# Optimization experiments

Measured on AMD Instinct MI355X. Metric: run time of the kernel, lower is better.

The kernel has to match this reference:

```python
import jax, jax.numpy as jnp
import numpy as np

N, C_IN, F = 64, 1024, 20          # batch, backbone channels, grid size (640/32)
N_CLASSES = 80
A = 3                               # anchors in this layer (mask [6,7,8])
STRIDE = 32
C = N_CLASSES + 5                   # 85
C_OUT = A * C                       # 255
ANCHORS = np.array([[116.0, 90.0], [156.0, 198.0], [373.0, 326.0]], np.float32) / STRIDE


def setup_inputs() -> dict:
    key = jax.random.key(0)
    k1, k2 = jax.random.split(key)
    xin = jax.random.normal(k1, (N, C_IN, F, F), jnp.float32)
    conv_w = jax.random.normal(k2, (C_OUT, C_IN, 1, 1), jnp.float32) * 0.02
    conv_b = jnp.zeros((C_OUT,), jnp.float32)
    return {"xin": xin, "conv_w": conv_w, "conv_b": conv_b}


def reference(xin, conv_w, conv_b):
    anchors = jnp.asarray(ANCHORS, dtype=xin.dtype)  # [A, 2], grid units
    # 1x1 conv head: [N, C_OUT, F, F]
    out = jax.lax.conv_general_dilated(xin, conv_w, window_strides=(1, 1),
                                       padding="VALID")
    out = out + conv_b[None, :, None, None]
    # [N, A, C, F, F] -> [N, A, F(y), F(x), C]
    out = out.reshape(N, A, C, F, F).transpose(0, 1, 3, 4, 2)

    xy = jax.nn.sigmoid(out[..., :2])       # sigmoid on tx, ty
    wh = out[..., 2:4]                      # raw tw, th
    objcls = jax.nn.sigmoid(out[..., 4:])   # sigmoid on obj + classes

    grid = jnp.arange(F, dtype=xin.dtype)
    px = xy[..., 0] + grid[None, None, None, :]   # + x_shift (varies along last spatial dim)
    py = xy[..., 1] + grid[None, None, :, None]   # + y_shift
    pw = jnp.exp(wh[..., 0]) * anchors[:, 0].reshape(1, A, 1, 1)
    ph = jnp.exp(wh[..., 1]) * anchors[:, 1].reshape(1, A, 1, 1)

    boxes = jnp.stack([px, py, pw, ph], axis=-1) * STRIDE  # back to pixel coords
    pred = jnp.concatenate([boxes, objcls], axis=-1)       # [N, A, F, F, C]
    return pred.reshape(N, -1, C)                           # [N, A*F*F, C]
```

## Files before the change

kernel.cpp:

```cpp
#include <hip/hip_runtime.h>
#include <hip/hip_bf16.h>
#include <math.h>

#define CIN    1024
#define S_TOT  400
#define COUT   255
#define NCH    85
#define NIMG   64
#define SB     16
#define NTHR   256

#define LDS_BYTES 16384

typedef __attribute__((ext_vector_type(8))) short bf16x8;
typedef __attribute__((ext_vector_type(4))) float f32x4;

struct __attribute__((aligned(4))) f4u { float x, y, z, w; };

__device__ __forceinline__ int xOff(int s, int gl) {
    return (s << 10) + ((gl << 4) ^ (((s >> 1) & 7) << 4));
}

__device__ __forceinline__ unsigned pk2(float a, float b) {
    __hip_bfloat162 h;
    h.x = __float2bfloat16(a);
    h.y = __float2bfloat16(b);
    return *reinterpret_cast<unsigned*>(&h);
}

__device__ __forceinline__ float sigmoidf_(float v) {
    return 1.0f / (1.0f + expf(-v));
}

__global__ __launch_bounds__(256) void w_pre2(const float* __restrict__ w,
                                              unsigned short* __restrict__ wbf) {
    int gidx = blockIdx.x * 256 + threadIdx.x;
    int co = gidx & 255;
    int g  = gidx >> 8;
    union { unsigned short u[8]; bf16x8 v; } pk;
    if (co < COUT) {
        const float* src = w + (size_t)co * CIN + g * 8;
        #pragma unroll
        for (int j = 0; j < 8; ++j) {
            __hip_bfloat16 h = __float2bfloat16(src[j]);
            pk.u[j] = *reinterpret_cast<unsigned short*>(&h);
        }
    } else {
        #pragma unroll
        for (int j = 0; j < 8; ++j) pk.u[j] = 0;
    }
    *reinterpret_cast<bf16x8*>((char*)wbf + ((size_t)(g << 8) + co) * 16) = pk.v;
}

__global__ __launch_bounds__(NTHR, 4) void yolo_mfma3(
    const float* __restrict__ xin,
    const unsigned short* __restrict__ wbf,
    const float* __restrict__ bias,
    float* __restrict__ out)
{
    __shared__ __align__(16) char smem[LDS_BYTES];

    const int sb  = blockIdx.x * SB;
    const int n   = blockIdx.y;
    const int tid = threadIdx.x;
    const int lane = tid & 63;
    const int wid  = tid >> 6;
    const int llo  = lane & 15;
    const int lhi  = lane >> 4;

    const int gl_u = tid >> 2;
    const int sq_u = tid & 3;

    f32x4 acc[4] = {};

    for (int h = 0; h < 2; ++h) {
        if (h) __syncthreads();

        {
            const float* src = xin
                + ((size_t)n * CIN + h * 512 + gl_u * 8) * S_TOT
                + sb + 4 * sq_u;
            float4 cu[8];
            #pragma unroll
            for (int j = 0; j < 8; ++j) cu[j] = *(const float4*)(src + j * S_TOT);
            union { unsigned u[4]; bf16x8 v; } rr;
            #pragma unroll
            for (int r = 0; r < 4; ++r) {
                const float* cf = (const float*)cu;
                #pragma unroll
                for (int j = 0; j < 4; ++j)
                    rr.u[j] = pk2(cf[8 * j + r], cf[8 * j + 4 + r]);
                *(bf16x8*)(smem + xOff(4 * sq_u + r, gl_u)) = rr.v;
            }
        }
        __syncthreads();

        #pragma unroll 4
        for (int kk = 0; kk < 16; ++kk) {
            const int gA = (h * 16 + kk) * 4 + lhi;
            const int gl = kk * 4 + lhi;
            bf16x8 b = *(bf16x8*)(smem + xOff(llo, gl));
            #pragma unroll
            for (int mi = 0; mi < 4; ++mi) {
                const int co = wid * 64 + mi * 16 + llo;
                bf16x8 a = *(const bf16x8*)((const char*)wbf
                                            + ((size_t)(gA << 8) + co) * 16);
                acc[mi] = __builtin_amdgcn_mfma_f32_16x16x32_bf16(a, b, acc[mi], 0, 0, 0);
            }
        }
    }

    const float anchW[3] = {116.0f, 156.0f, 373.0f};
    const float anchH[3] = {90.0f, 198.0f, 326.0f};

    const int s = sb + llo;
    const float sx = (float)(s % 20);
    const float sy = (float)(s / 20);

    #pragma unroll
    for (int mi = 0; mi < 4; ++mi) {
        const int co0 = wid * 64 + mi * 16 + lhi * 4;
        const int aW  = co0 / NCH;
        const int c0  = co0 - aW * NCH;
        const bool whole = (c0 <= NCH - 4) && (co0 + 3 < COUT);
        float bv[4];
        #pragma unroll
        for (int r = 0; r < 4; ++r)
            bv[r] = (co0 + r < COUT) ? bias[co0 + r] : 0.0f;

        if (whole) {
            float r4[4];
            #pragma unroll
            for (int r = 0; r < 4; ++r) {
                const int c = c0 + r;
                const float v = acc[mi][r] + bv[r];
                float res;
                if (c == 0)      res = (sigmoidf_(v) + sx) * 32.0f;
                else if (c == 1) res = (sigmoidf_(v) + sy) * 32.0f;
                else if (c == 2) res = expf(v) * anchW[aW];
                else if (c == 3) res = expf(v) * anchH[aW];
                else             res = sigmoidf_(v);
                r4[r] = res;
            }
            f4u* p = (f4u*)(out + (size_t)n * 102000 + aW * 34000 + s * 85 + c0);
            f4u val = {r4[0], r4[1], r4[2], r4[3]};
            *p = val;
        } else {
            #pragma unroll
            for (int r = 0; r < 4; ++r) {
                const int co = co0 + r;
                if (co < COUT) {
                    const int a2 = co / NCH;
                    const int c  = co - a2 * NCH;
                    const float v = acc[mi][r] + bv[r];
                    float res;
                    if (c == 0)      res = (sigmoidf_(v) + sx) * 32.0f;
                    else if (c == 1) res = (sigmoidf_(v) + sy) * 32.0f;
                    else if (c == 2) res = expf(v) * anchW[a2];
                    else if (c == 3) res = expf(v) * anchH[a2];
                    else             res = sigmoidf_(v);
                    out[(size_t)n * 102000 + a2 * 34000 + s * 85 + c] = res;
                }
            }
        }
    }
}

extern "C" void kernel_launch(void* const* d_in, const int* in_sizes, int n_in,
                              void* d_out, int out_size, void* d_ws, size_t ws_size,
                              hipStream_t stream) {
    const float* xin  = (const float*)d_in[0];
    const float* w    = (const float*)d_in[1];
    const float* bias = (const float*)d_in[2];
    float* out = (float*)d_out;
    unsigned short* wbf = (unsigned short*)d_ws;

    w_pre2<<<128, 256, 0, stream>>>(w, wbf);
    yolo_mfma3<<<dim3(S_TOT / SB, NIMG), NTHR, 0, stream>>>(xin, wbf, bias, out);
}
```

Before: 77.23 us.

## Stage full K tile in LDS once and software-pipeline MFMA operand loads

The kernel now loads the whole 1024-channel input slice for the block into a 32 KB LDS buffer in one pass, where before it used two 512-channel halves separated by a barrier. The MFMA loop is restructured to prefetch the next iteration's LDS B operand and global weight A operands while the current MFMAs issue. This removes one barrier and is meant to hide weight-load latency behind compute. In exchange it doubles LDS per block, which may reduce occupancy, and it raises register pressure from the double-buffered operands.

Result: faster. 72.50 us (-6.1%).

```diff
diff --git a/kernel.cpp b/kernel.cpp
--- a/kernel.cpp
+++ b/kernel.cpp
@@ -10,15 +10,15 @@
 #define SB     16
 #define NTHR   256
 
-#define LDS_BYTES 16384
+#define LDS_BYTES 32768
 
 typedef __attribute__((ext_vector_type(8))) short bf16x8;
 typedef __attribute__((ext_vector_type(4))) float f32x4;
 
 struct __attribute__((aligned(4))) f4u { float x, y, z, w; };
 
-__device__ __forceinline__ int xOff(int s, int gl) {
-    return (s << 10) + ((gl << 4) ^ (((s >> 1) & 7) << 4));
+__device__ __forceinline__ int xOff(int s, int g) {
+    return (s << 11) + ((g << 4) ^ (((s >> 1) & 7) << 4));
 }
 
 __device__ __forceinline__ unsigned pk2(float a, float b) {
@@ -52,7 +52,7 @@
     *reinterpret_cast<bf16x8*>((char*)wbf + ((size_t)(g << 8) + co) * 16) = pk.v;
 }
 
-__global__ __launch_bounds__(NTHR, 4) void yolo_mfma3(
+__global__ __launch_bounds__(NTHR, 4) void yolo_mfma4(
     const float* __restrict__ xin,
     const unsigned short* __restrict__ wbf,
     const float* __restrict__ bias,
@@ -68,47 +68,55 @@
     const int llo  = lane & 15;
     const int lhi  = lane >> 4;
 
-    const int gl_u = tid >> 2;
-    const int sq_u = tid & 3;
+    #pragma unroll
+    for (int p = 0; p < 2; ++p) {
+        const int u   = p * 256 + tid;
+        const int g_u = u >> 2;
+        const int sq  = u & 3;
+        const float* src = xin + ((size_t)n * CIN + g_u * 8) * S_TOT + sb + 4 * sq;
+        float4 cu[8];
+        #pragma unroll
+        for (int j = 0; j < 8; ++j) cu[j] = *(const float4*)(src + j * S_TOT);
+        const float* cf = (const float*)cu;
+        #pragma unroll
+        for (int r = 0; r < 4; ++r) {
+            union { unsigned u4[4]; bf16x8 v; } rr;
+            #pragma unroll
+            for (int j = 0; j < 4; ++j)
+                rr.u4[j] = pk2(cf[8 * j + r], cf[8 * j + 4 + r]);
+            *(bf16x8*)(smem + xOff(4 * sq + r, g_u)) = rr.v;
+        }
+    }
+    __syncthreads();
 
     f32x4 acc[4] = {};
+    const char* wb = (const char*)wbf;
+    const int coB = wid * 64 + llo;
 
-    for (int h = 0; h < 2; ++h) {
-        if (h) __syncthreads();
+    bf16x8 b_c = *(bf16x8*)(smem + xOff(llo, lhi));
+    bf16x8 a_c[4];
+    #pragma unroll
+    for (int mi = 0; mi < 4; ++mi)
+        a_c[mi] = *(const bf16x8*)(wb + ((size_t)((lhi << 8) + coB + mi * 16)) * 16);
 
-        {
-            const float* src = xin
-                + ((size_t)n * CIN + h * 512 + gl_u * 8) * S_TOT
-                + sb + 4 * sq_u;
-            float4 cu[8];
-            #pragma unroll
-            for (int j = 0; j < 8; ++j) cu[j] = *(const float4*)(src + j * S_TOT);
-            union { unsigned u[4]; bf16x8 v; } rr;
-            #pragma unroll
-            for (int r = 0; r < 4; ++r) {
-                const float* cf = (const float*)cu;
-                #pragma unroll
-                for (int j = 0; j < 4; ++j)
-                    rr.u[j] = pk2(cf[8 * j + r], cf[8 * j + 4 + r]);
-                *(bf16x8*)(smem + xOff(4 * sq_u + r, gl_u)) = rr.v;
-            }
-        }
-        __syncthreads();
-
-        #pragma unroll 4
-        for (int kk = 0; kk < 16; ++kk) {
-            const int gA = (h * 16 + kk) * 4 + lhi;
-            const int gl = kk * 4 + lhi;
-            bf16x8 b = *(bf16x8*)(smem + xOff(llo, gl));
-            #pragma unroll
-            for (int mi = 0; mi < 4; ++mi) {
-                const int co = wid * 64 + mi * 16 + llo;
-                bf16x8 a = *(const bf16x8*)((const char*)wbf
-                                            + ((size_t)(gA << 8) + co) * 16);
-                acc[mi] = __builtin_amdgcn_mfma_f32_16x16x32_bf16(a, b, acc[mi], 0, 0, 0);
-            }
-        }
+    #pragma unroll 4
+    for (int kk = 0; kk < 31; ++kk) {
+        const int gn = (kk + 1) * 4 + lhi;
+        bf16x8 b_n = *(bf16x8*)(smem + xOff(llo, gn));
+        bf16x8 a_n[4];
+        #pragma unroll
+        for (int mi = 0; mi < 4; ++mi)
+            a_n[mi] = *(const bf16x8*)(wb + ((size_t)((gn << 8) + coB + mi * 16)) * 16);
+        #pragma unroll
+        for (int mi = 0; mi < 4; ++mi)
+            acc[mi] = __builtin_amdgcn_mfma_f32_16x16x32_bf16(a_c[mi], b_c, acc[mi], 0, 0, 0);
+        b_c = b_n;
+        #pragma unroll
+        for (int mi = 0; mi < 4; ++mi) a_c[mi] = a_n[mi];
     }
+    #pragma unroll
+    for (int mi = 0; mi < 4; ++mi)
+        acc[mi] = __builtin_amdgcn_mfma_f32_16x16x32_bf16(a_c[mi], b_c, acc[mi], 0, 0, 0);
 
     const float anchW[3] = {116.0f, 156.0f, 373.0f};
     const float anchH[3] = {90.0f, 198.0f, 326.0f};
@@ -176,5 +184,5 @@
     unsigned short* wbf = (unsigned short*)d_ws;
 
     w_pre2<<<128, 256, 0, stream>>>(w, wbf);
-    yolo_mfma3<<<dim3(S_TOT / SB, NIMG), NTHR, 0, stream>>>(xin, wbf, bias, out);
+    yolo_mfma4<<<dim3(S_TOT / SB, NIMG), NTHR, 0, stream>>>(xin, wbf, bias, out);
 }
```

## Flatten batch-spatial tiling to 64 positions per block with double-buffered LDS pipeline

Applied to the files above, without the earlier changes.

Flattens the batch and spatial dims into one index and gives each 512-thread block 64 positions across all output channels, so every weight fragment load feeds four MFMAs instead of one. The K dimension is split into four phases with double-buffered LDS: the next phase's global loads are issued before the current MFMAs and written to the other buffer afterwards, with one barrier per phase. This cuts weight traffic per block and overlaps input loads with compute. The cost is more registers (8 accumulators plus staging), 64KB of LDS and fewer, larger blocks. Tiles of 64 positions can span an image boundary, so the epilogue works out n and s for each position.

Result: faster. 69.22 us (-10.4%).

```diff
diff --git a/kernel.cpp b/kernel.cpp
--- a/kernel.cpp
+++ b/kernel.cpp
@@ -7,18 +7,23 @@
 #define COUT   255
 #define NCH    85
 #define NIMG   64
-#define SB     16
-#define NTHR   256
-
-#define LDS_BYTES 16384
+#define NFLAT  (NIMG * S_TOT)
+#define TS     64
+#define NTHR   512
+#define NPH    4
+#define KPH    256
+#define GPH    32
+
+#define XBUF_B    32768
+#define LDS_BYTES (2 * XBUF_B)
 
 typedef __attribute__((ext_vector_type(8))) short bf16x8;
 typedef __attribute__((ext_vector_type(4))) float f32x4;
 
 struct __attribute__((aligned(4))) f4u { float x, y, z, w; };
 
-__device__ __forceinline__ int xOff(int s, int gl) {
-    return (s << 10) + ((gl << 4) ^ (((s >> 1) & 7) << 4));
+__device__ __forceinline__ int xoff0(int s, int g) {
+    return (s << 9) + ((g << 4) ^ (((s ^ (s >> 3)) & 7) << 4));
 }
 
 __device__ __forceinline__ unsigned pk2(float a, float b) {
@@ -36,10 +41,10 @@
                                               unsigned short* __restrict__ wbf) {
     int gidx = blockIdx.x * 256 + threadIdx.x;
     int co = gidx & 255;
-    int g  = gidx >> 8;
+    int gg = gidx >> 8;
     union { unsigned short u[8]; bf16x8 v; } pk;
     if (co < COUT) {
-        const float* src = w + (size_t)co * CIN + g * 8;
+        const float* src = w + (size_t)co * CIN + gg * 8;
         #pragma unroll
         for (int j = 0; j < 8; ++j) {
             __hip_bfloat16 h = __float2bfloat16(src[j]);
@@ -49,10 +54,10 @@
         #pragma unroll
         for (int j = 0; j < 8; ++j) pk.u[j] = 0;
     }
-    *reinterpret_cast<bf16x8*>((char*)wbf + ((size_t)(g << 8) + co) * 16) = pk.v;
-}
-
-__global__ __launch_bounds__(NTHR, 4) void yolo_mfma3(
+    *reinterpret_cast<bf16x8*>((char*)wbf + ((size_t)(gg << 8) + co) * 16) = pk.v;
+}
+
+__global__ __launch_bounds__(NTHR, 4) void yolo_ws(
     const float* __restrict__ xin,
     const unsigned short* __restrict__ wbf,
     const float* __restrict__ bias,
@@ -60,52 +65,78 @@
 {
     __shared__ __align__(16) char smem[LDS_BYTES];
 
-    const int sb  = blockIdx.x * SB;
-    const int n   = blockIdx.y;
-    const int tid = threadIdx.x;
+    const int tile = blockIdx.x * TS;
+    const int tid  = threadIdx.x;
     const int lane = tid & 63;
-    const int wid  = tid >> 6;
+    const int w    = tid >> 6;
     const int llo  = lane & 15;
     const int lhi  = lane >> 4;
 
-    const int gl_u = tid >> 2;
-    const int sq_u = tid & 3;
-
-    f32x4 acc[4] = {};
-
-    for (int h = 0; h < 2; ++h) {
-        if (h) __syncthreads();
-
-        {
-            const float* src = xin
-                + ((size_t)n * CIN + h * 512 + gl_u * 8) * S_TOT
-                + sb + 4 * sq_u;
-            float4 cu[8];
-            #pragma unroll
-            for (int j = 0; j < 8; ++j) cu[j] = *(const float4*)(src + j * S_TOT);
-            union { unsigned u[4]; bf16x8 v; } rr;
+    const int flat_l = tile + 4 * llo;
+    const int n_l = flat_l / S_TOT;
+    const int s_l = flat_l - n_l * S_TOT;
+    const float* xbase = xin + (size_t)n_l * (CIN * S_TOT) + s_l;
+    const int ci_row = w * 32 + lhi * 8;
+    const int g_loc  = w * 4 + lhi;
+
+    f32x4 acc[2][4] = {};
+    union F4 { float4 v; float f[4]; };
+    F4 st[8];
+
+    {
+        const float* src = xbase + (size_t)ci_row * S_TOT;
+        #pragma unroll
+        for (int j = 0; j < 8; ++j) st[j].v = *(const float4*)(src + j * S_TOT);
+        #pragma unroll
+        for (int r = 0; r < 4; ++r) {
+            union { unsigned u4[4]; bf16x8 b; } rr;
+            #pragma unroll
+            for (int jj = 0; jj < 4; ++jj)
+                rr.u4[jj] = pk2(st[2 * jj].f[r], st[2 * jj + 1].f[r]);
+            *(bf16x8*)(smem + xoff0(4 * llo + r, g_loc)) = rr.b;
+        }
+    }
+
+    for (int p = 0; p < NPH; ++p) {
+        if (p + 1 < NPH) {
+            const float* src = xbase + (size_t)((p + 1) * KPH + ci_row) * S_TOT;
+            #pragma unroll
+            for (int j = 0; j < 8; ++j) st[j].v = *(const float4*)(src + j * S_TOT);
+        }
+        __builtin_amdgcn_sched_barrier(0);
+        asm volatile("s_waitcnt lgkmcnt(0)" ::: "memory");
+        __builtin_amdgcn_s_barrier();
+        __builtin_amdgcn_sched_barrier(0);
+
+        const char* xb = smem + (p & 1) * XBUF_B;
+        #pragma unroll
+        for (int step = 0; step < 8; ++step) {
+            const int gl = step * 4 + lhi;
+            bf16x8 bfr[4];
+            #pragma unroll
+            for (int ns = 0; ns < 4; ++ns)
+                bfr[ns] = *(const bf16x8*)(xb + xoff0(ns * 16 + llo, gl));
+            #pragma unroll
+            for (int mi = 0; mi < 2; ++mi) {
+                const int co = w * 32 + mi * 16 + llo;
+                bf16x8 a = *(const bf16x8*)((const char*)wbf
+                            + ((size_t)(((p * GPH + gl) << 8) + co)) * 16);
+                #pragma unroll
+                for (int ns = 0; ns < 4; ++ns)
+                    acc[mi][ns] = __builtin_amdgcn_mfma_f32_16x16x32_bf16(
+                        a, bfr[ns], acc[mi][ns], 0, 0, 0);
+            }
+        }
+
+        if (p + 1 < NPH) {
+            char* xb2 = smem + ((p + 1) & 1) * XBUF_B;
             #pragma unroll
             for (int r = 0; r < 4; ++r) {
-                const float* cf = (const float*)cu;
-                #pragma unroll
-                for (int j = 0; j < 4; ++j)
-                    rr.u[j] = pk2(cf[8 * j + r], cf[8 * j + 4 + r]);
-                *(bf16x8*)(smem + xOff(4 * sq_u + r, gl_u)) = rr.v;
-            }
-        }
-        __syncthreads();
-
-        #pragma unroll 4
-        for (int kk = 0; kk < 16; ++kk) {
-            const int gA = (h * 16 + kk) * 4 + lhi;
-            const int gl = kk * 4 + lhi;
-            bf16x8 b = *(bf16x8*)(smem + xOff(llo, gl));
-            #pragma unroll
-            for (int mi = 0; mi < 4; ++mi) {
-                const int co = wid * 64 + mi * 16 + llo;
-                bf16x8 a = *(const bf16x8*)((const char*)wbf
-                                            + ((size_t)(gA << 8) + co) * 16);
-                acc[mi] = __builtin_amdgcn_mfma_f32_16x16x32_bf16(a, b, acc[mi], 0, 0, 0);
+                union { unsigned u4[4]; bf16x8 b; } rr;
+                #pragma unroll
+                for (int jj = 0; jj < 4; ++jj)
+                    rr.u4[jj] = pk2(st[2 * jj].f[r], st[2 * jj + 1].f[r]);
+                *(bf16x8*)(xb2 + xoff0(4 * llo + r, g_loc)) = rr.b;
             }
         }
     }
@@ -113,13 +144,9 @@
     const float anchW[3] = {116.0f, 156.0f, 373.0f};
     const float anchH[3] = {90.0f, 198.0f, 326.0f};
 
-    const int s = sb + llo;
-    const float sx = (float)(s % 20);
-    const float sy = (float)(s / 20);
-
     #pragma unroll
-    for (int mi = 0; mi < 4; ++mi) {
-        const int co0 = wid * 64 + mi * 16 + lhi * 4;
+    for (int mi = 0; mi < 2; ++mi) {
+        const int co0 = w * 32 + mi * 16 + lhi * 4;
         const int aW  = co0 / NCH;
         const int c0  = co0 - aW * NCH;
         const bool whole = (c0 <= NCH - 4) && (co0 + 3 < COUT);
@@ -128,38 +155,46 @@
         for (int r = 0; r < 4; ++r)
             bv[r] = (co0 + r < COUT) ? bias[co0 + r] : 0.0f;
 
-        if (whole) {
-            float r4[4];
-            #pragma unroll
-            for (int r = 0; r < 4; ++r) {
-                const int c = c0 + r;
-                const float v = acc[mi][r] + bv[r];
-                float res;
-                if (c == 0)      res = (sigmoidf_(v) + sx) * 32.0f;
-                else if (c == 1) res = (sigmoidf_(v) + sy) * 32.0f;
-                else if (c == 2) res = expf(v) * anchW[aW];
-                else if (c == 3) res = expf(v) * anchH[aW];
-                else             res = sigmoidf_(v);
-                r4[r] = res;
-            }
-            f4u* p = (f4u*)(out + (size_t)n * 102000 + aW * 34000 + s * 85 + c0);
-            f4u val = {r4[0], r4[1], r4[2], r4[3]};
-            *p = val;
-        } else {
-            #pragma unroll
-            for (int r = 0; r < 4; ++r) {
-                const int co = co0 + r;
-                if (co < COUT) {
-                    const int a2 = co / NCH;
-                    const int c  = co - a2 * NCH;
-                    const float v = acc[mi][r] + bv[r];
+        #pragma unroll
+        for (int ns = 0; ns < 4; ++ns) {
+            const int flat = tile + ns * 16 + llo;
+            const int n = flat / S_TOT;
+            const int s = flat - n * S_TOT;
+            const float sx = (float)(s % 20);
+            const float sy = (float)(s / 20);
+            if (whole) {
+                float r4[4];
+                #pragma unroll
+                for (int r = 0; r < 4; ++r) {
+                    const int c = c0 + r;
+                    const float v = acc[mi][ns][r] + bv[r];
                     float res;
                     if (c == 0)      res = (sigmoidf_(v) + sx) * 32.0f;
                     else if (c == 1) res = (sigmoidf_(v) + sy) * 32.0f;
-                    else if (c == 2) res = expf(v) * anchW[a2];
-                    else if (c == 3) res = expf(v) * anchH[a2];
+                    else if (c == 2) res = expf(v) * anchW[aW];
+                    else if (c == 3) res = expf(v) * anchH[aW];
                     else             res = sigmoidf_(v);
-                    out[(size_t)n * 102000 + a2 * 34000 + s * 85 + c] = res;
+                    r4[r] = res;
+                }
+                f4u* pp = (f4u*)(out + (size_t)n * 102000 + aW * 34000 + s * 85 + c0);
+                f4u val = {r4[0], r4[1], r4[2], r4[3]};
+                *pp = val;
+            } else {
+                #pragma unroll
+                for (int r = 0; r < 4; ++r) {
+                    const int co = co0 + r;
+                    if (co < COUT) {
+                        const int a2 = co / NCH;
+                        const int c  = co - a2 * NCH;
+                        const float v = acc[mi][ns][r] + bv[r];
+                        float res;
+                        if (c == 0)      res = (sigmoidf_(v) + sx) * 32.0f;
+                        else if (c == 1) res = (sigmoidf_(v) + sy) * 32.0f;
+                        else if (c == 2) res = expf(v) * anchW[a2];
+                        else if (c == 3) res = expf(v) * anchH[a2];
+                        else             res = sigmoidf_(v);
+                        out[(size_t)n * 102000 + a2 * 34000 + s * 85 + c] = res;
+                    }
                 }
             }
         }
@@ -176,5 +211,5 @@
     unsigned short* wbf = (unsigned short*)d_ws;
 
     w_pre2<<<128, 256, 0, stream>>>(w, wbf);
-    yolo_mfma3<<<dim3(S_TOT / SB, NIMG), NTHR, 0, stream>>>(xin, wbf, bias, out);
-}
+    yolo_ws<<<NFLAT / TS, NTHR, 0, stream>>>(xin, wbf, bias, out);
+}
```
